# Kernel tuning notes

Hardware: AMD Instinct MI355X
Metric: run time of the kernel (lower is better)

## Reference

```python
import jax, jax.numpy as jnp
import numpy as np

B, S, DIM = 2, 2048, 2048
H, KVH, D = 16, 8, 128
EPS = 1e-6
ROPE_BASE = 1000000.0
MAX_SEQ = 8192


def _build_rope(max_seq, dim, base):
    inv_freq = 1.0 / (base ** (np.arange(0, dim, 2, dtype=np.float64) / dim))
    t = np.arange(max_seq, dtype=np.float64)
    freqs = np.outer(t, inv_freq)  # [max_seq, dim//2]
    return (jnp.asarray(np.cos(freqs), jnp.float32),
            jnp.asarray(np.sin(freqs), jnp.float32))


def setup_inputs() -> dict:
    key = jax.random.key(0)
    ks = jax.random.split(key, 7)
    scale = 0.02
    cos_cache, sin_cache = _build_rope(MAX_SEQ, D, ROPE_BASE)
    return {
        "x": jax.random.normal(ks[0], (B, S, DIM), jnp.float32),
        "wq": jax.random.normal(ks[1], (DIM, H * D), jnp.float32) * scale,
        "wk": jax.random.normal(ks[2], (DIM, KVH * D), jnp.float32) * scale,
        "wv": jax.random.normal(ks[3], (DIM, KVH * D), jnp.float32) * scale,
        "wo": jax.random.normal(ks[4], (H * D, DIM), jnp.float32) * scale,
        "q_gamma": 1.0 + 0.01 * jax.random.normal(ks[5], (D,), jnp.float32),
        "k_gamma": 1.0 + 0.01 * jax.random.normal(ks[6], (D,), jnp.float32),
        "cos_cache": cos_cache,
        "sin_cache": sin_cache,
    }


def _rmsnorm(t, gamma):
    var = jnp.mean(t * t, axis=-1, keepdims=True)
    return t * jax.lax.rsqrt(var + EPS) * gamma


def _rotate_half(t):
    t1, t2 = jnp.split(t, 2, axis=-1)
    return jnp.concatenate((-t2, t1), axis=-1)


def _apply_rope(t, cos, sin):
    # t: [B, S, heads, D]; cos/sin: [S, D//2]
    cos_f = jnp.concatenate((cos, cos), axis=-1)[None, :, None, :]
    sin_f = jnp.concatenate((sin, sin), axis=-1)[None, :, None, :]
    return t * cos_f + _rotate_half(t) * sin_f


def reference(x, wq, wk, wv, wo, q_gamma, k_gamma, cos_cache, sin_cache):
    b, s, _ = x.shape
    q = (x @ wq).reshape(b, s, H, D)
    k = (x @ wk).reshape(b, s, KVH, D)
    v = (x @ wv).reshape(b, s, KVH, D)
    q = _rmsnorm(q, q_gamma)
    k = _rmsnorm(k, k_gamma)
    # prefill: kv_len == q_len == s, cache empty
    cos, sin = cos_cache[:s], sin_cache[:s]
    q = _apply_rope(q, cos, sin)
    k = _apply_rope(k, cos, sin)
    # -> [B, heads, S, D]
    q = q.transpose(0, 2, 1, 3)
    k = k.transpose(0, 2, 1, 3)
    v = v.transpose(0, 2, 1, 3)
    # GQA: repeat_interleave kv heads
    g = H // KVH
    k = jnp.repeat(k, g, axis=1)
    v = jnp.repeat(v, g, axis=1)
    scale = 1.0 / jnp.sqrt(jnp.asarray(D, x.dtype))
    scores = jnp.einsum("bhqd,bhkd->bhqk", q, k) * scale
    causal = jnp.tril(jnp.ones((s, s), bool))
    scores = jnp.where(causal, scores, jnp.finfo(scores.dtype).min)
    attn = jax.nn.softmax(scores, axis=-1)
    out = jnp.einsum("bhqk,bhkd->bhqd", attn, v)
    out = out.transpose(0, 2, 1, 3).reshape(b, s, H * D)
    return out @ wo
```

## Files before the change

kernel.cpp:

```cpp
#include <hip/hip_runtime.h>
#include <hip/hip_bf16.h>


typedef __attribute__((ext_vector_type(8))) short s16x8;
typedef __attribute__((ext_vector_type(4))) float f32x4;
typedef __attribute__((ext_vector_type(16))) float f32x16;

typedef const __attribute__((address_space(1))) void* gas_t;
typedef __attribute__((address_space(3))) void* las_t;
#define GLL16(g, l) __builtin_amdgcn_global_load_lds((gas_t)(const void*)(g), (las_t)(void*)(l), 16, 0, 0)

static __device__ __forceinline__ unsigned short f2bf(float f) {
    union { float f; unsigned u; } v; v.f = f;
    unsigned r = v.u + 0x7FFF + ((v.u >> 16) & 1);
    return (unsigned short)(r >> 16);
}
static __device__ __forceinline__ float bf2f(unsigned short h) {
    union { unsigned u; float f; } v; v.u = ((unsigned)h) << 16;
    return v.f;
}
static __device__ __forceinline__ float exp2_fast(float x) {
    float r; asm("v_exp_f32 %0, %1" : "=v"(r) : "v"(x)); return r;
}
static __device__ __forceinline__ unsigned cvt_pk_bf16(float a, float b) {
    unsigned r; asm("v_cvt_pk_bf16_f32 %0, %1, %2" : "=v"(r) : "v"(a), "v"(b)); return r;
}

#define SCALE_L2E 0.12751744900929f

__global__ __launch_bounds__(256) void k_convert_x(const float* __restrict__ x,
                                                   unsigned short* __restrict__ xb, int n) {
    int i = (blockIdx.x * 256 + threadIdx.x) * 8;
    if (i >= n) return;
    float4 a = *(const float4*)(x + i);
    float4 b = *(const float4*)(x + i + 4);
    s16x8 o;
    o[0] = (short)f2bf(a.x); o[1] = (short)f2bf(a.y); o[2] = (short)f2bf(a.z); o[3] = (short)f2bf(a.w);
    o[4] = (short)f2bf(b.x); o[5] = (short)f2bf(b.y); o[6] = (short)f2bf(b.z); o[7] = (short)f2bf(b.w);
    *(s16x8*)(xb + i) = o;
}

__global__ __launch_bounds__(256) void k_transpose_w(const float* __restrict__ src,
                                                     unsigned short* __restrict__ dst,
                                                     int K, int N, int nbase, int dstld) {
    __shared__ float t[32][33];
    int k0 = blockIdx.x * 32, n0 = blockIdx.y * 32;
    int tx = threadIdx.x & 31, ty0 = threadIdx.x >> 5;
    for (int p = 0; p < 4; p++) {
        int ty = ty0 + p * 8;
        t[ty][tx] = src[(size_t)(k0 + ty) * N + n0 + tx];
    }
    __syncthreads();
    for (int p = 0; p < 4; p++) {
        int ty = ty0 + p * 8;
        dst[(size_t)(nbase + n0 + ty) * dstld + k0 + tx] = f2bf(t[tx][ty]);
    }
}

__global__ __launch_bounds__(256) void k_transpose_v(const unsigned short* __restrict__ V,
                                                     unsigned short* __restrict__ Vt) {
    __shared__ unsigned short t[32][33];
    int s0 = blockIdx.x * 32, d0 = blockIdx.y * 32;
    size_t base = (size_t)blockIdx.z * 2048 * 128;
    int tx = threadIdx.x & 31, ty0 = threadIdx.x >> 5;
    for (int p = 0; p < 4; p++) {
        int ty = ty0 + p * 8;
        t[ty][tx] = V[base + (size_t)(s0 + ty) * 128 + d0 + tx];
    }
    __syncthreads();
    for (int p = 0; p < 4; p++) {
        int ty = ty0 + p * 8;
        Vt[base + (size_t)(d0 + ty) * 2048 + s0 + tx] = t[tx][ty];
    }
}

template<int OUTF32>
__global__ __launch_bounds__(512, 2) void k_gemm256(const unsigned short* __restrict__ A,
                                                    const unsigned short* __restrict__ Bt,
                                                    void* __restrict__ Cout,
                                                    int M, int N, int K) {
    __shared__ unsigned short Ls[2][2][2][8192];
    int tid = threadIdx.x, lane = tid & 63, wave = tid >> 6;
    int wm = wave >> 2, wn = wave & 3;
    int lr = lane & 15, lg = lane >> 4;
    int swrow = wave * 16 + (lane >> 2);
    int scol  = (((lane & 3) ^ ((lane >> 3) & 3)) * 8);
    int cg    = ((lg ^ ((lr >> 1) & 3)) * 8);
    const unsigned short* Ab = A  + (size_t)(blockIdx.x * 256) * K;
    const unsigned short* Bb = Bt + (size_t)(blockIdx.y * 256) * K;

    f32x4 acc[8][4] = {};
    int NK = K / 64;

    auto issue = [&](int slot, int mat, int kk, int k0) {
        const unsigned short* base = mat ? Bb : Ab;
        unsigned short* dst = &Ls[slot][mat][kk][wave * 512];
        GLL16(base + (size_t)swrow * K + k0 + kk * 32 + scol, dst);
        GLL16(base + (size_t)(swrow + 128) * K + k0 + kk * 32 + scol, dst + 4096);
    };

    issue(0, 0, 0, 0);
    issue(0, 1, 0, 0);
    issue(0, 0, 1, 0);
    issue(0, 1, 1, 0);
    asm volatile("s_waitcnt vmcnt(4)" ::: "memory");
    __builtin_amdgcn_s_barrier();

    for (int t = 0; t < NK; ++t) {
        int slot = t & 1, nslot = slot ^ 1;
        int kn = (t + 1) * 64;
        bool more = (t + 1) < NK;
        const unsigned short* As0 = Ls[slot][0][0];
        const unsigned short* Bs0 = Ls[slot][1][0];
        const unsigned short* As1 = Ls[slot][0][1];
        const unsigned short* Bs1 = Ls[slot][1][1];
        s16x8 af[4], bfr[4];

        #pragma unroll
        for (int m = 0; m < 4; m++) af[m]  = *(const s16x8*)&As0[(wm * 128 + m * 16 + lr) * 32 + cg];
        #pragma unroll
        for (int n = 0; n < 4; n++) bfr[n] = *(const s16x8*)&Bs0[(wn * 64 + n * 16 + lr) * 32 + cg];
        if (more) issue(nslot, 0, 0, kn);
        asm volatile("" ::: "memory");
        __builtin_amdgcn_s_barrier();
        __builtin_amdgcn_s_setprio(1);
        #pragma unroll
        for (int m = 0; m < 4; m++)
            #pragma unroll
            for (int n = 0; n < 4; n++)
                acc[m][n] = __builtin_amdgcn_mfma_f32_16x16x32_bf16(af[m], bfr[n], acc[m][n], 0, 0, 0);
        __builtin_amdgcn_s_setprio(0);
        asm volatile("" ::: "memory");
        __builtin_amdgcn_s_barrier();

        #pragma unroll
        for (int m = 0; m < 4; m++) af[m] = *(const s16x8*)&As0[(wm * 128 + (m + 4) * 16 + lr) * 32 + cg];
        if (more) { issue(nslot, 1, 0, kn); asm volatile("s_waitcnt vmcnt(4)" ::: "memory"); }
        else      {                         asm volatile("s_waitcnt vmcnt(0)" ::: "memory"); }
        asm volatile("" ::: "memory");
        __builtin_amdgcn_s_barrier();
        __builtin_amdgcn_s_setprio(1);
        #pragma unroll
        for (int m = 0; m < 4; m++)
            #pragma unroll
            for (int n = 0; n < 4; n++)
                acc[m + 4][n] = __builtin_amdgcn_mfma_f32_16x16x32_bf16(af[m], bfr[n], acc[m + 4][n], 0, 0, 0);
        __builtin_amdgcn_s_setprio(0);
        asm volatile("" ::: "memory");
        __builtin_amdgcn_s_barrier();

        #pragma unroll
        for (int m = 0; m < 4; m++) af[m]  = *(const s16x8*)&As1[(wm * 128 + m * 16 + lr) * 32 + cg];
        #pragma unroll
        for (int n = 0; n < 4; n++) bfr[n] = *(const s16x8*)&Bs1[(wn * 64 + n * 16 + lr) * 32 + cg];
        if (more) issue(nslot, 0, 1, kn);
        asm volatile("" ::: "memory");
        __builtin_amdgcn_s_barrier();
        __builtin_amdgcn_s_setprio(1);
        #pragma unroll
        for (int m = 0; m < 4; m++)
            #pragma unroll
            for (int n = 0; n < 4; n++)
                acc[m][n] = __builtin_amdgcn_mfma_f32_16x16x32_bf16(af[m], bfr[n], acc[m][n], 0, 0, 0);
        __builtin_amdgcn_s_setprio(0);
        asm volatile("" ::: "memory");
        __builtin_amdgcn_s_barrier();

        #pragma unroll
        for (int m = 0; m < 4; m++) af[m] = *(const s16x8*)&As1[(wm * 128 + (m + 4) * 16 + lr) * 32 + cg];
        if (more) { issue(nslot, 1, 1, kn); asm volatile("s_waitcnt vmcnt(4)" ::: "memory"); }
        asm volatile("" ::: "memory");
        __builtin_amdgcn_s_barrier();
        __builtin_amdgcn_s_setprio(1);
        #pragma unroll
        for (int m = 0; m < 4; m++)
            #pragma unroll
            for (int n = 0; n < 4; n++)
                acc[m + 4][n] = __builtin_amdgcn_mfma_f32_16x16x32_bf16(af[m], bfr[n], acc[m + 4][n], 0, 0, 0);
        __builtin_amdgcn_s_setprio(0);
        asm volatile("" ::: "memory");
        __builtin_amdgcn_s_barrier();
    }

    int rbase = blockIdx.x * 256 + wm * 128;
    int cbase = blockIdx.y * 256 + wn * 64;
    #pragma unroll
    for (int am = 0; am < 8; am++)
        #pragma unroll
        for (int n = 0; n < 4; n++)
            #pragma unroll
            for (int r = 0; r < 4; r++) {
                int row = rbase + am * 16 + lg * 4 + r;
                int col = cbase + n * 16 + lr;
                float v = acc[am][n][r];
                if (OUTF32) ((float*)Cout)[(size_t)row * N + col] = v;
                else        ((unsigned short*)Cout)[(size_t)row * N + col] = f2bf(v);
            }
}

template<int OUTF32>
__global__ __launch_bounds__(256) void k_gemm_bt(const unsigned short* __restrict__ A,
                                                 const unsigned short* __restrict__ Bt,
                                                 void* __restrict__ Cout,
                                                 int M, int N, int K) {
    __shared__ unsigned short As[128 * 32];
    __shared__ unsigned short Bs[128 * 32];
    int tid = threadIdx.x;
    int lane = tid & 63;
    int wave = tid >> 6;
    int wm = wave >> 1, wn = wave & 1;
    int lr = lane & 15, lk = (lane >> 4) * 8;
    int srow = wave * 32 + (lane >> 2);
    int scol = (lane & 3) * 8;
    const unsigned short* Ag0 = A  + (size_t)(blockIdx.x * 128 + srow) * K + scol;
    const unsigned short* Ag1 = Ag0 + (size_t)16 * K;
    const unsigned short* Bg0 = Bt + (size_t)(blockIdx.y * 128 + srow) * K + scol;
    const unsigned short* Bg1 = Bg0 + (size_t)16 * K;
    unsigned short* Asw = &As[wave * 1024];
    unsigned short* Bsw = &Bs[wave * 1024];
    f32x4 acc[4][4] = {};
    for (int k0 = 0; k0 < K; k0 += 32) {
        __syncthreads();
        GLL16(Ag0 + k0, Asw);
        GLL16(Ag1 + k0, Asw + 512);
        GLL16(Bg0 + k0, Bsw);
        GLL16(Bg1 + k0, Bsw + 512);
        __syncthreads();
        s16x8 af[4], bfr[4];
        #pragma unroll
        for (int m = 0; m < 4; m++) af[m]  = *(const s16x8*)&As[(wm * 64 + m * 16 + lr) * 32 + lk];
        #pragma unroll
        for (int n = 0; n < 4; n++) bfr[n] = *(const s16x8*)&Bs[(wn * 64 + n * 16 + lr) * 32 + lk];
        #pragma unroll
        for (int m = 0; m < 4; m++)
            #pragma unroll
            for (int n = 0; n < 4; n++)
                acc[m][n] = __builtin_amdgcn_mfma_f32_16x16x32_bf16(af[m], bfr[n], acc[m][n], 0, 0, 0);
    }
    int rbase = blockIdx.x * 128 + wm * 64;
    int cbase = blockIdx.y * 128 + wn * 64;
    #pragma unroll
    for (int m = 0; m < 4; m++)
        #pragma unroll
        for (int n = 0; n < 4; n++)
            #pragma unroll
            for (int r = 0; r < 4; r++) {
                int row = rbase + m * 16 + (lane >> 4) * 4 + r;
                int col = cbase + n * 16 + lr;
                float v = acc[m][n][r];
                if (OUTF32) ((float*)Cout)[(size_t)row * N + col] = v;
                else        ((unsigned short*)Cout)[(size_t)row * N + col] = f2bf(v);
            }
}

__global__ __launch_bounds__(256) void k_rms_rope(const unsigned short* __restrict__ qkv,
                                                  const float* __restrict__ qg,
                                                  const float* __restrict__ kg,
                                                  const float* __restrict__ cosc,
                                                  const float* __restrict__ sinc,
                                                  unsigned short* __restrict__ Qt,
                                                  unsigned short* __restrict__ Kt,
                                                  unsigned short* __restrict__ Vt) {
    int r = blockIdx.x;
    int b = r >> 11;
    int s = r & 2047;
    int tid = threadIdx.x;
    int wave = tid >> 6, lane = tid & 63;
    int sl = lane >> 4;
    int li = lane & 15;
    int d0 = li * 8;
    const unsigned short* row = qkv + (size_t)r * 4096;
    #pragma unroll
    for (int p = 0; p < 2; p++) {
        int seg = p * 16 + wave * 4 + sl;
        s16x8 raw = *(const s16x8*)(row + seg * 128 + d0);
        if (seg >= 24) {
            *(s16x8*)(Vt + ((size_t)(b * 8 + (seg - 24)) * 2048 + s) * 128 + d0) = raw;
            continue;
        }
        float e[8];
        #pragma unroll
        for (int j = 0; j < 8; j++) e[j] = bf2f((unsigned short)raw[j]);
        float ssq = 0.f;
        #pragma unroll
        for (int j = 0; j < 8; j++) ssq += e[j] * e[j];
        ssq += __shfl_xor(ssq, 1, 64);
        ssq += __shfl_xor(ssq, 2, 64);
        ssq += __shfl_xor(ssq, 4, 64);
        ssq += __shfl_xor(ssq, 8, 64);
        float rn = rsqrtf(ssq * (1.0f / 128.0f) + 1e-6f);
        const float* g = (seg < 16) ? qg : kg;
        float gs = (seg < 16) ? SCALE_L2E : 1.0f;
        float4 g0 = *(const float4*)(g + d0);
        float4 g1 = *(const float4*)(g + d0 + 4);
        float t[8];
        t[0] = e[0] * rn * g0.x * gs; t[1] = e[1] * rn * g0.y * gs;
        t[2] = e[2] * rn * g0.z * gs; t[3] = e[3] * rn * g0.w * gs;
        t[4] = e[4] * rn * g1.x * gs; t[5] = e[5] * rn * g1.y * gs;
        t[6] = e[6] * rn * g1.z * gs; t[7] = e[7] * rn * g1.w * gs;
        float pr[8];
        #pragma unroll
        for (int j = 0; j < 8; j++) pr[j] = __shfl_xor(t[j], 8, 64);
        int didx = d0 & 63;
        float4 c0 = *(const float4*)(cosc + (size_t)s * 64 + didx);
        float4 c1 = *(const float4*)(cosc + (size_t)s * 64 + didx + 4);
        float4 sn0 = *(const float4*)(sinc + (size_t)s * 64 + didx);
        float4 sn1 = *(const float4*)(sinc + (size_t)s * 64 + didx + 4);
        float cv[8] = {c0.x, c0.y, c0.z, c0.w, c1.x, c1.y, c1.z, c1.w};
        float sv[8] = {sn0.x, sn0.y, sn0.z, sn0.w, sn1.x, sn1.y, sn1.z, sn1.w};
        float sgn = (li < 8) ? -1.0f : 1.0f;
        s16x8 o;
        #pragma unroll
        for (int j = 0; j < 8; j++)
            o[j] = (short)f2bf(t[j] * cv[j] + sgn * pr[j] * sv[j]);
        unsigned short* dst = (seg < 16)
            ? Qt + ((size_t)(b * 16 + seg) * 2048 + s) * 128 + d0
            : Kt + ((size_t)(b * 8 + (seg - 16)) * 2048 + s) * 128 + d0;
        *(s16x8*)dst = o;
    }
}

__global__ __launch_bounds__(256, 2) void k_attn(const unsigned short* __restrict__ Qt,
                                                 const unsigned short* __restrict__ Kt,
                                                 const unsigned short* __restrict__ Vtg,
                                                 unsigned short* __restrict__ attn) {
    __shared__ unsigned short Ks[64][136];
    __shared__ unsigned short Vs[128][72];
    __shared__ unsigned short Ps[4][32][72];
    int bid = blockIdx.x;
    int lo = bid & 255;
    int qb, bh;
    if (bid < 256) { qb = lo & 15;        bh = lo >> 4; }
    else           { qb = 15 - (lo & 15); bh = 16 + (lo >> 4); }
    int b = bh >> 4, h = bh & 15;
    int kvh = h >> 1;
    int tid = threadIdx.x;
    int lane = tid & 63, wave = tid >> 6;
    int ql = lane & 31;
    int hf = lane >> 5;
    int q0 = qb * 128;
    const unsigned short* Qb    = Qt + ((size_t)bh * 2048 + q0 + wave * 32 + ql) * 128;
    const unsigned short* Kbase = Kt + (size_t)(b * 8 + kvh) * 2048 * 128;
    const unsigned short* Vtb   = Vtg + (size_t)(b * 8 + kvh) * 128 * 2048;
    s16x8 aq[8];
    #pragma unroll
    for (int ds = 0; ds < 8; ds++)
        aq[ds] = *(const s16x8*)(Qb + ds * 16 + hf * 8);
    f32x16 out[4] = {};
    float m_q = -1e30f, l_q = 0.f;
    int qglob = q0 + wave * 32 + ql;
    int qlo   = q0 + wave * 32;
    int qhi   = qlo + 31;
    int ntiles = 2 * qb + 2;
    int krow = tid >> 4, kcol = (tid & 15) * 8;
    int vrow = tid >> 3, vcol = (tid & 7) * 8;
    s16x8 kpre[4], vpre[4];
    #pragma unroll
    for (int p = 0; p < 4; p++) {
        kpre[p] = *(const s16x8*)(Kbase + (size_t)(krow + p * 16) * 128 + kcol);
        vpre[p] = *(const s16x8*)(Vtb + (size_t)(vrow + p * 32) * 2048 + vcol);
    }

    for (int t = 0; t < ntiles; t++) {
        int k0 = t * 64;
        __syncthreads();
        #pragma unroll
        for (int p = 0; p < 4; p++) {
            *(s16x8*)&Ks[krow + p * 16][kcol] = kpre[p];
            *(s16x8*)&Vs[vrow + p * 32][vcol] = vpre[p];
        }
        __syncthreads();
        if (t + 1 < ntiles) {
            int kn = k0 + 64;
            #pragma unroll
            for (int p = 0; p < 4; p++) {
                kpre[p] = *(const s16x8*)(Kbase + (size_t)(kn + krow + p * 16) * 128 + kcol);
                vpre[p] = *(const s16x8*)(Vtb + (size_t)(vrow + p * 32) * 2048 + kn + vcol);
            }
        }
        if (k0 <= qhi) {
            f32x16 st[2] = {};
            __builtin_amdgcn_s_setprio(1);
            #pragma unroll
            for (int sub = 0; sub < 2; sub++)
                #pragma unroll
                for (int ds = 0; ds < 8; ds++) {
                    s16x8 kf = *(const s16x8*)&Ks[sub * 32 + ql][ds * 16 + hf * 8];
                    st[sub] = __builtin_amdgcn_mfma_f32_32x32x16_bf16(kf, aq[ds], st[sub], 0, 0, 0);
                }
            __builtin_amdgcn_s_setprio(0);
            float mx = -1e30f;
            if (k0 + 63 > qlo) {
                #pragma unroll
                for (int sub = 0; sub < 2; sub++)
                    #pragma unroll
                    for (int r = 0; r < 16; r++) {
                        int kv = k0 + sub * 32 + (r & 3) + 8 * (r >> 2) + 4 * hf;
                        if (kv > qglob) st[sub][r] = -1e30f;
                        mx = fmaxf(mx, st[sub][r]);
                    }
            } else {
                #pragma unroll
                for (int sub = 0; sub < 2; sub++)
                    #pragma unroll
                    for (int r = 0; r < 16; r++) mx = fmaxf(mx, st[sub][r]);
            }
            mx = fmaxf(mx, __shfl_xor(mx, 32, 64));
            bool defer = __all(mx <= m_q + 8.0f);
            float sf = 1.0f;
            if (!defer) {
                float mnew = fmaxf(m_q, mx);
                sf = exp2_fast(m_q - mnew);
                m_q = mnew;
            }
            float rs = 0.f;
            #pragma unroll
            for (int sub = 0; sub < 2; sub++)
                #pragma unroll
                for (int r = 0; r < 16; r++) {
                    float e = exp2_fast(st[sub][r] - m_q);
                    st[sub][r] = e;
                    rs += e;
                }
            rs += __shfl_xor(rs, 32, 64);
            l_q = defer ? (l_q + rs) : (l_q * sf + rs);
            #pragma unroll
            for (int sub = 0; sub < 2; sub++)
                #pragma unroll
                for (int g = 0; g < 4; g++) {
                    uint2 w;
                    w.x = cvt_pk_bf16(st[sub][4 * g + 0], st[sub][4 * g + 1]);
                    w.y = cvt_pk_bf16(st[sub][4 * g + 2], st[sub][4 * g + 3]);
                    *(uint2*)&Ps[wave][ql][sub * 32 + g * 8 + hf * 4] = w;
                }
            if (!defer) {
                float sfr[16];
                #pragma unroll
                for (int r = 0; r < 16; r++)
                    sfr[r] = __shfl(sf, (r & 3) + 8 * (r >> 2) + 4 * hf, 64);
                #pragma unroll
                for (int dblk = 0; dblk < 4; dblk++)
                    #pragma unroll
                    for (int r = 0; r < 16; r++) out[dblk][r] *= sfr[r];
            }
            __builtin_amdgcn_s_setprio(1);
            #pragma unroll
            for (int ks = 0; ks < 4; ks++) {
                s16x8 pf = *(const s16x8*)&Ps[wave][ql][ks * 16 + hf * 8];
                #pragma unroll
                for (int dblk = 0; dblk < 4; dblk++) {
                    s16x8 vf = *(const s16x8*)&Vs[dblk * 32 + ql][ks * 16 + hf * 8];
                    out[dblk] = __builtin_amdgcn_mfma_f32_32x32x16_bf16(pf, vf, out[dblk], 0, 0, 0);
                }
            }
            __builtin_amdgcn_s_setprio(0);
        }
    }
    float linv = 1.0f / l_q;
    float inv[16];
    #pragma unroll
    for (int r = 0; r < 16; r++)
        inv[r] = __shfl(linv, (r & 3) + 8 * (r >> 2) + 4 * hf, 64);
    #pragma unroll
    for (int dblk = 0; dblk < 4; dblk++)
        #pragma unroll
        for (int r = 0; r < 16; r++) {
            int row = q0 + wave * 32 + (r & 3) + 8 * (r >> 2) + 4 * hf;
            attn[((size_t)(b * 2048) + row) * 2048 + h * 128 + dblk * 32 + ql] =
                f2bf(out[dblk][r] * inv[r]);
        }
}

extern "C" void kernel_launch(void* const* d_in, const int* in_sizes, int n_in,
                              void* d_out, int out_size, void* d_ws, size_t ws_size,
                              hipStream_t stream) {
    const float* x    = (const float*)d_in[0];
    const float* wq   = (const float*)d_in[1];
    const float* wk   = (const float*)d_in[2];
    const float* wv   = (const float*)d_in[3];
    const float* wo   = (const float*)d_in[4];
    const float* qg   = (const float*)d_in[5];
    const float* kg   = (const float*)d_in[6];
    const float* cosc = (const float*)d_in[7];
    const float* sinc = (const float*)d_in[8];

    char* ws = (char*)d_ws;
    unsigned short* xb   = (unsigned short*)(ws);
    unsigned short* w1t  = (unsigned short*)(ws + 16777216);
    unsigned short* w2t  = (unsigned short*)(ws + 33554432);
    unsigned short* qkv  = (unsigned short*)(ws + 41943040);
    unsigned short* Qt   = (unsigned short*)(ws + 75497472);
    unsigned short* Kt   = (unsigned short*)(ws + 92274688);
    unsigned short* Vt   = (unsigned short*)(ws + 100663296);
    unsigned short* attn = (unsigned short*)(ws + 109051904);
    unsigned short* Vtg  = qkv;

    k_convert_x<<<4096, 256, 0, stream>>>(x, xb, 8388608);
    k_transpose_w<<<dim3(64, 64), 256, 0, stream>>>(wq, w1t, 2048, 2048, 0, 2048);
    k_transpose_w<<<dim3(64, 32), 256, 0, stream>>>(wk, w1t, 2048, 1024, 2048, 2048);
    k_transpose_w<<<dim3(64, 32), 256, 0, stream>>>(wv, w1t, 2048, 1024, 3072, 2048);
    k_transpose_w<<<dim3(64, 64), 256, 0, stream>>>(wo, w2t, 2048, 2048, 0, 2048);
    k_gemm256<0><<<dim3(16, 16), 512, 0, stream>>>(xb, w1t, qkv, 4096, 4096, 2048);
    k_rms_rope<<<4096, 256, 0, stream>>>(qkv, qg, kg, cosc, sinc, Qt, Kt, Vt);
    k_transpose_v<<<dim3(64, 4, 16), 256, 0, stream>>>(Vt, Vtg);
    k_attn<<<512, 256, 0, stream>>>(Qt, Kt, Vtg, attn);
    k_gemm_bt<1><<<dim3(32, 16), 256, 0, stream>>>(attn, w2t, d_out, 4096, 2048, 2048);
}
```

Before: 226.8 us.

## Split attention into single-wave blocks loading K/V straight to registers

Restructures the attention kernel so each block is one 64-thread wave handling 32 queries, launching 2048 blocks instead of 512. K and V fragments are now loaded directly from global memory into registers with software prefetch, which removes the shared-memory staging and block-wide barriers. The block index mapping is also changed to interleave heads and order query chunks in a snake pattern for load balance and L2 locality. The trade-off is losing K/V reuse across the four waves that shared a tile, so global/L2 traffic rises and register pressure goes up from the 16-register K prefetch.

```diff
diff --git a/kernel.cpp b/kernel.cpp
--- a/kernel.cpp
+++ b/kernel.cpp
@@ -320,26 +320,23 @@
     }
 }
 
-__global__ __launch_bounds__(256, 2) void k_attn(const unsigned short* __restrict__ Qt,
-                                                 const unsigned short* __restrict__ Kt,
-                                                 const unsigned short* __restrict__ Vtg,
-                                                 unsigned short* __restrict__ attn) {
-    __shared__ unsigned short Ks[64][136];
-    __shared__ unsigned short Vs[128][72];
-    __shared__ unsigned short Ps[4][32][72];
+__global__ __launch_bounds__(64, 2) void k_attn(const unsigned short* __restrict__ Qt,
+                                                const unsigned short* __restrict__ Kt,
+                                                const unsigned short* __restrict__ Vtg,
+                                                unsigned short* __restrict__ attn) {
+    __shared__ unsigned short Ps[32][72];
     int bid = blockIdx.x;
-    int lo = bid & 255;
-    int qb, bh;
-    if (bid < 256) { qb = lo & 15;        bh = lo >> 4; }
-    else           { qb = 15 - (lo & 15); bh = 16 + (lo >> 4); }
+    int x = bid & 7, l = bid >> 3;
+    int bh = x * 4 + (l & 3);
+    int cc = (l >> 2) & 7, j = l >> 5;
+    int qc = j * 8 + ((j & 1) ? (7 - cc) : cc);
     int b = bh >> 4, h = bh & 15;
     int kvh = h >> 1;
-    int tid = threadIdx.x;
-    int lane = tid & 63, wave = tid >> 6;
+    int lane = threadIdx.x;
     int ql = lane & 31;
     int hf = lane >> 5;
-    int q0 = qb * 128;
-    const unsigned short* Qb    = Qt + ((size_t)bh * 2048 + q0 + wave * 32 + ql) * 128;
+    int q0 = qc * 32;
+    const unsigned short* Qb    = Qt + ((size_t)bh * 2048 + q0 + ql) * 128;
     const unsigned short* Kbase = Kt + (size_t)(b * 8 + kvh) * 2048 * 128;
     const unsigned short* Vtb   = Vtg + (size_t)(b * 8 + kvh) * 128 * 2048;
     s16x8 aq[8];
@@ -348,113 +345,115 @@
         aq[ds] = *(const s16x8*)(Qb + ds * 16 + hf * 8);
     f32x16 out[4] = {};
     float m_q = -1e30f, l_q = 0.f;
-    int qglob = q0 + wave * 32 + ql;
-    int qlo   = q0 + wave * 32;
-    int qhi   = qlo + 31;
-    int ntiles = 2 * qb + 2;
-    int krow = tid >> 4, kcol = (tid & 15) * 8;
-    int vrow = tid >> 3, vcol = (tid & 7) * 8;
-    s16x8 kpre[4], vpre[4];
-    #pragma unroll
-    for (int p = 0; p < 4; p++) {
-        kpre[p] = *(const s16x8*)(Kbase + (size_t)(krow + p * 16) * 128 + kcol);
-        vpre[p] = *(const s16x8*)(Vtb + (size_t)(vrow + p * 32) * 2048 + vcol);
-    }
+    int qglob = q0 + ql;
+    int ntiles = (qc >> 1) + 1;
+    s16x8 kreg[16];
+    #pragma unroll
+    for (int sub = 0; sub < 2; sub++)
+        #pragma unroll
+        for (int ds = 0; ds < 8; ds++)
+            kreg[sub * 8 + ds] = *(const s16x8*)(Kbase + (size_t)(sub * 32 + ql) * 128 + ds * 16 + hf * 8);
 
     for (int t = 0; t < ntiles; t++) {
         int k0 = t * 64;
-        __syncthreads();
-        #pragma unroll
-        for (int p = 0; p < 4; p++) {
-            *(s16x8*)&Ks[krow + p * 16][kcol] = kpre[p];
-            *(s16x8*)&Vs[vrow + p * 32][vcol] = vpre[p];
-        }
-        __syncthreads();
+        f32x16 st[2] = {};
+        __builtin_amdgcn_s_setprio(1);
+        #pragma unroll
+        for (int sub = 0; sub < 2; sub++)
+            #pragma unroll
+            for (int ds = 0; ds < 8; ds++)
+                st[sub] = __builtin_amdgcn_mfma_f32_32x32x16_bf16(kreg[sub * 8 + ds], aq[ds], st[sub], 0, 0, 0);
+        __builtin_amdgcn_s_setprio(0);
         if (t + 1 < ntiles) {
             int kn = k0 + 64;
             #pragma unroll
-            for (int p = 0; p < 4; p++) {
-                kpre[p] = *(const s16x8*)(Kbase + (size_t)(kn + krow + p * 16) * 128 + kcol);
-                vpre[p] = *(const s16x8*)(Vtb + (size_t)(vrow + p * 32) * 2048 + kn + vcol);
-            }
-        }
-        if (k0 <= qhi) {
-            f32x16 st[2] = {};
-            __builtin_amdgcn_s_setprio(1);
-            #pragma unroll
             for (int sub = 0; sub < 2; sub++)
                 #pragma unroll
-                for (int ds = 0; ds < 8; ds++) {
-                    s16x8 kf = *(const s16x8*)&Ks[sub * 32 + ql][ds * 16 + hf * 8];
-                    st[sub] = __builtin_amdgcn_mfma_f32_32x32x16_bf16(kf, aq[ds], st[sub], 0, 0, 0);
-                }
-            __builtin_amdgcn_s_setprio(0);
-            float mx = -1e30f;
-            if (k0 + 63 > qlo) {
-                #pragma unroll
-                for (int sub = 0; sub < 2; sub++)
-                    #pragma unroll
-                    for (int r = 0; r < 16; r++) {
-                        int kv = k0 + sub * 32 + (r & 3) + 8 * (r >> 2) + 4 * hf;
-                        if (kv > qglob) st[sub][r] = -1e30f;
-                        mx = fmaxf(mx, st[sub][r]);
-                    }
-            } else {
-                #pragma unroll
-                for (int sub = 0; sub < 2; sub++)
-                    #pragma unroll
-                    for (int r = 0; r < 16; r++) mx = fmaxf(mx, st[sub][r]);
-            }
-            mx = fmaxf(mx, __shfl_xor(mx, 32, 64));
-            bool defer = __all(mx <= m_q + 8.0f);
-            float sf = 1.0f;
-            if (!defer) {
-                float mnew = fmaxf(m_q, mx);
-                sf = exp2_fast(m_q - mnew);
-                m_q = mnew;
-            }
-            float rs = 0.f;
+                for (int ds = 0; ds < 8; ds++)
+                    kreg[sub * 8 + ds] = *(const s16x8*)(Kbase + (size_t)(kn + sub * 32 + ql) * 128 + ds * 16 + hf * 8);
+        }
+        s16x8 vA[8];
+        #pragma unroll
+        for (int ks = 0; ks < 2; ks++)
+            #pragma unroll
+            for (int dblk = 0; dblk < 4; dblk++)
+                vA[ks * 4 + dblk] = *(const s16x8*)(Vtb + (size_t)(dblk * 32 + ql) * 2048 + k0 + ks * 16 + hf * 8);
+        float mx = -1e30f;
+        if (k0 + 63 > q0) {
             #pragma unroll
             for (int sub = 0; sub < 2; sub++)
                 #pragma unroll
                 for (int r = 0; r < 16; r++) {
-                    float e = exp2_fast(st[sub][r] - m_q);
-                    st[sub][r] = e;
-                    rs += e;
+                    int kv = k0 + sub * 32 + (r & 3) + 8 * (r >> 2) + 4 * hf;
+                    if (kv > qglob) st[sub][r] = -1e30f;
+                    mx = fmaxf(mx, st[sub][r]);
                 }
-            rs += __shfl_xor(rs, 32, 64);
-            l_q = defer ? (l_q + rs) : (l_q * sf + rs);
+        } else {
             #pragma unroll
             for (int sub = 0; sub < 2; sub++)
                 #pragma unroll
-                for (int g = 0; g < 4; g++) {
-                    uint2 w;
-                    w.x = cvt_pk_bf16(st[sub][4 * g + 0], st[sub][4 * g + 1]);
-                    w.y = cvt_pk_bf16(st[sub][4 * g + 2], st[sub][4 * g + 3]);
-                    *(uint2*)&Ps[wave][ql][sub * 32 + g * 8 + hf * 4] = w;
-                }
-            if (!defer) {
-                float sfr[16];
+                for (int r = 0; r < 16; r++) mx = fmaxf(mx, st[sub][r]);
+        }
+        mx = fmaxf(mx, __shfl_xor(mx, 32, 64));
+        bool defer = __all(mx <= m_q + 8.0f);
+        float sf = 1.0f;
+        if (!defer) {
+            float mnew = fmaxf(m_q, mx);
+            sf = exp2_fast(m_q - mnew);
+            m_q = mnew;
+        }
+        float rs = 0.f;
+        #pragma unroll
+        for (int sub = 0; sub < 2; sub++)
+            #pragma unroll
+            for (int r = 0; r < 16; r++) {
+                float e = exp2_fast(st[sub][r] - m_q);
+                st[sub][r] = e;
+                rs += e;
+            }
+        rs += __shfl_xor(rs, 32, 64);
+        l_q = defer ? (l_q + rs) : (l_q * sf + rs);
+        #pragma unroll
+        for (int sub = 0; sub < 2; sub++)
+            #pragma unroll
+            for (int g = 0; g < 4; g++) {
+                uint2 w;
+                w.x = cvt_pk_bf16(st[sub][4 * g + 0], st[sub][4 * g + 1]);
+                w.y = cvt_pk_bf16(st[sub][4 * g + 2], st[sub][4 * g + 3]);
+                *(uint2*)&Ps[ql][sub * 32 + g * 8 + hf * 4] = w;
+            }
+        s16x8 vB[8];
+        #pragma unroll
+        for (int ks = 0; ks < 2; ks++)
+            #pragma unroll
+            for (int dblk = 0; dblk < 4; dblk++)
+                vB[ks * 4 + dblk] = *(const s16x8*)(Vtb + (size_t)(dblk * 32 + ql) * 2048 + k0 + (ks + 2) * 16 + hf * 8);
+        if (!defer) {
+            float sfr[16];
+            #pragma unroll
+            for (int r = 0; r < 16; r++)
+                sfr[r] = __shfl(sf, (r & 3) + 8 * (r >> 2) + 4 * hf, 64);
+            #pragma unroll
+            for (int dblk = 0; dblk < 4; dblk++)
                 #pragma unroll
-                for (int r = 0; r < 16; r++)
-                    sfr[r] = __shfl(sf, (r & 3) + 8 * (r >> 2) + 4 * hf, 64);
-                #pragma unroll
-                for (int dblk = 0; dblk < 4; dblk++)
-                    #pragma unroll
-                    for (int r = 0; r < 16; r++) out[dblk][r] *= sfr[r];
-            }
-            __builtin_amdgcn_s_setprio(1);
-            #pragma unroll
-            for (int ks = 0; ks < 4; ks++) {
-                s16x8 pf = *(const s16x8*)&Ps[wave][ql][ks * 16 + hf * 8];
-                #pragma unroll
-                for (int dblk = 0; dblk < 4; dblk++) {
-                    s16x8 vf = *(const s16x8*)&Vs[dblk * 32 + ql][ks * 16 + hf * 8];
-                    out[dblk] = __builtin_amdgcn_mfma_f32_32x32x16_bf16(pf, vf, out[dblk], 0, 0, 0);
-                }
-            }
-            __builtin_amdgcn_s_setprio(0);
-        }
+                for (int r = 0; r < 16; r++) out[dblk][r] *= sfr[r];
+        }
+        __builtin_amdgcn_s_setprio(1);
+        #pragma unroll
+        for (int ks = 0; ks < 2; ks++) {
+            s16x8 pf = *(const s16x8*)&Ps[ql][ks * 16 + hf * 8];
+            #pragma unroll
+            for (int dblk = 0; dblk < 4; dblk++)
+                out[dblk] = __builtin_amdgcn_mfma_f32_32x32x16_bf16(pf, vA[ks * 4 + dblk], out[dblk], 0, 0, 0);
+        }
+        #pragma unroll
+        for (int ks = 0; ks < 2; ks++) {
+            s16x8 pf = *(const s16x8*)&Ps[ql][(ks + 2) * 16 + hf * 8];
+            #pragma unroll
+            for (int dblk = 0; dblk < 4; dblk++)
+                out[dblk] = __builtin_amdgcn_mfma_f32_32x32x16_bf16(pf, vB[ks * 4 + dblk], out[dblk], 0, 0, 0);
+        }
+        __builtin_amdgcn_s_setprio(0);
     }
     float linv = 1.0f / l_q;
     float inv[16];
@@ -465,7 +464,7 @@
     for (int dblk = 0; dblk < 4; dblk++)
         #pragma unroll
         for (int r = 0; r < 16; r++) {
-            int row = q0 + wave * 32 + (r & 3) + 8 * (r >> 2) + 4 * hf;
+            int row = q0 + (r & 3) + 8 * (r >> 2) + 4 * hf;
             attn[((size_t)(b * 2048) + row) * 2048 + h * 128 + dblk * 32 + ql] =
                 f2bf(out[dblk][r] * inv[r]);
         }
@@ -503,6 +502,6 @@
     k_gemm256<0><<<dim3(16, 16), 512, 0, stream>>>(xb, w1t, qkv, 4096, 4096, 2048);
     k_rms_rope<<<4096, 256, 0, stream>>>(qkv, qg, kg, cosc, sinc, Qt, Kt, Vt);
     k_transpose_v<<<dim3(64, 4, 16), 256, 0, stream>>>(Vt, Vtg);
-    k_attn<<<512, 256, 0, stream>>>(Qt, Kt, Vtg, attn);
+    k_attn<<<2048, 64, 0, stream>>>(Qt, Kt, Vtg, attn);
     k_gemm_bt<1><<<dim3(32, 16), 256, 0, stream>>>(attn, w2t, d_out, 4096, 2048, 2048);
 }
```

Result: slower. 297.2 us (+31.0%).

## Use 4-stage LDS ring in QKV GEMM and merge weight transposes into one launch

Applied to the files above, without the earlier changes.

The 256x256 GEMM moves from a double-buffered 64-wide K step with four barrier-separated phases to a four-slot ring of 32-wide K slices. Loads are issued three slices ahead, and there are two barriers per 32-wide slice. This is meant to hide global-load latency better and cut synchronisation per unit of work. The four weight-transpose launches are merged into one 3D-grid launch, with early exit for the shorter wk and wv matrices, to save launch overhead. The ring keeps the same total LDS, but its vmcnt accounting is more intricate and easier to get wrong.

```diff
diff --git a/kernel.cpp b/kernel.cpp
--- a/kernel.cpp
+++ b/kernel.cpp
@@ -40,11 +40,21 @@
     *(s16x8*)(xb + i) = o;
 }
 
-__global__ __launch_bounds__(256) void k_transpose_w(const float* __restrict__ src,
-                                                     unsigned short* __restrict__ dst,
-                                                     int K, int N, int nbase, int dstld) {
+__global__ __launch_bounds__(256) void k_transpose_w4(const float* __restrict__ wq,
+                                                      const float* __restrict__ wk,
+                                                      const float* __restrict__ wv,
+                                                      const float* __restrict__ wo,
+                                                      unsigned short* __restrict__ w1t,
+                                                      unsigned short* __restrict__ w2t) {
     __shared__ float t[32][33];
+    int z = blockIdx.z;
+    const float* src; unsigned short* dst; int N, nbase;
+    if (z == 0)      { src = wq; dst = w1t; N = 2048; nbase = 0;    }
+    else if (z == 1) { src = wk; dst = w1t; N = 1024; nbase = 2048; }
+    else if (z == 2) { src = wv; dst = w1t; N = 1024; nbase = 3072; }
+    else             { src = wo; dst = w2t; N = 2048; nbase = 0;    }
     int k0 = blockIdx.x * 32, n0 = blockIdx.y * 32;
+    if (n0 >= N) return;
     int tx = threadIdx.x & 31, ty0 = threadIdx.x >> 5;
     for (int p = 0; p < 4; p++) {
         int ty = ty0 + p * 8;
@@ -53,7 +63,7 @@
     __syncthreads();
     for (int p = 0; p < 4; p++) {
         int ty = ty0 + p * 8;
-        dst[(size_t)(nbase + n0 + ty) * dstld + k0 + tx] = f2bf(t[tx][ty]);
+        dst[(size_t)(nbase + n0 + ty) * 2048 + k0 + tx] = f2bf(t[tx][ty]);
     }
 }
 
@@ -79,7 +89,7 @@
                                                     const unsigned short* __restrict__ Bt,
                                                     void* __restrict__ Cout,
                                                     int M, int N, int K) {
-    __shared__ unsigned short Ls[2][2][2][8192];
+    __shared__ unsigned short Ls[4 * 2 * 8192];
     int tid = threadIdx.x, lane = tid & 63, wave = tid >> 6;
     int wm = wave >> 2, wn = wave & 3;
     int lr = lane & 15, lg = lane >> 4;
@@ -90,39 +100,41 @@
     const unsigned short* Bb = Bt + (size_t)(blockIdx.y * 256) * K;
 
     f32x4 acc[8][4] = {};
-    int NK = K / 64;
-
-    auto issue = [&](int slot, int mat, int kk, int k0) {
+    int NK = K / 32;
+
+    auto issue = [&](int ring, int mat, int k0) {
         const unsigned short* base = mat ? Bb : Ab;
-        unsigned short* dst = &Ls[slot][mat][kk][wave * 512];
-        GLL16(base + (size_t)swrow * K + k0 + kk * 32 + scol, dst);
-        GLL16(base + (size_t)(swrow + 128) * K + k0 + kk * 32 + scol, dst + 4096);
+        unsigned short* dst = &Ls[(ring * 2 + mat) * 8192 + wave * 512];
+        GLL16(base + (size_t)swrow * K + k0 + scol, dst);
+        GLL16(base + (size_t)(swrow + 128) * K + k0 + scol, dst + 4096);
     };
 
-    issue(0, 0, 0, 0);
-    issue(0, 1, 0, 0);
-    issue(0, 0, 1, 0);
-    issue(0, 1, 1, 0);
-    asm volatile("s_waitcnt vmcnt(4)" ::: "memory");
+    issue(0, 0, 0);  issue(0, 1, 0);
+    issue(1, 0, 32); issue(1, 1, 32);
+    issue(2, 0, 64); issue(2, 1, 64);
+    asm volatile("s_waitcnt vmcnt(8)" ::: "memory");
     __builtin_amdgcn_s_barrier();
+    asm volatile("" ::: "memory");
 
     for (int t = 0; t < NK; ++t) {
-        int slot = t & 1, nslot = slot ^ 1;
-        int kn = (t + 1) * 64;
-        bool more = (t + 1) < NK;
-        const unsigned short* As0 = Ls[slot][0][0];
-        const unsigned short* Bs0 = Ls[slot][1][0];
-        const unsigned short* As1 = Ls[slot][0][1];
-        const unsigned short* Bs1 = Ls[slot][1][1];
+        int ring = t & 3;
+        const unsigned short* As = &Ls[(ring * 2 + 0) * 8192];
+        const unsigned short* Bs = &Ls[(ring * 2 + 1) * 8192];
         s16x8 af[4], bfr[4];
-
-        #pragma unroll
-        for (int m = 0; m < 4; m++) af[m]  = *(const s16x8*)&As0[(wm * 128 + m * 16 + lr) * 32 + cg];
-        #pragma unroll
-        for (int n = 0; n < 4; n++) bfr[n] = *(const s16x8*)&Bs0[(wn * 64 + n * 16 + lr) * 32 + cg];
-        if (more) issue(nslot, 0, 0, kn);
+        #pragma unroll
+        for (int m = 0; m < 4; m++) af[m]  = *(const s16x8*)&As[(wm * 128 + m * 16 + lr) * 32 + cg];
+        #pragma unroll
+        for (int n = 0; n < 4; n++) bfr[n] = *(const s16x8*)&Bs[(wn * 64 + n * 16 + lr) * 32 + cg];
+        int rem = NK - 1 - t;
+        if (rem >= 3) {
+            int kn = (t + 3) * 32, rn = (t + 3) & 3;
+            issue(rn, 0, kn); issue(rn, 1, kn);
+        }
+        if (rem >= 3)      asm volatile("s_waitcnt vmcnt(8)" ::: "memory");
+        else if (rem == 2) asm volatile("s_waitcnt vmcnt(4)" ::: "memory");
+        else if (rem == 1) asm volatile("s_waitcnt vmcnt(0)" ::: "memory");
+        __builtin_amdgcn_s_barrier();
         asm volatile("" ::: "memory");
-        __builtin_amdgcn_s_barrier();
         __builtin_amdgcn_s_setprio(1);
         #pragma unroll
         for (int m = 0; m < 4; m++)
@@ -130,15 +142,8 @@
             for (int n = 0; n < 4; n++)
                 acc[m][n] = __builtin_amdgcn_mfma_f32_16x16x32_bf16(af[m], bfr[n], acc[m][n], 0, 0, 0);
         __builtin_amdgcn_s_setprio(0);
-        asm volatile("" ::: "memory");
-        __builtin_amdgcn_s_barrier();
-
-        #pragma unroll
-        for (int m = 0; m < 4; m++) af[m] = *(const s16x8*)&As0[(wm * 128 + (m + 4) * 16 + lr) * 32 + cg];
-        if (more) { issue(nslot, 1, 0, kn); asm volatile("s_waitcnt vmcnt(4)" ::: "memory"); }
-        else      {                         asm volatile("s_waitcnt vmcnt(0)" ::: "memory"); }
-        asm volatile("" ::: "memory");
-        __builtin_amdgcn_s_barrier();
+        #pragma unroll
+        for (int m = 0; m < 4; m++) af[m] = *(const s16x8*)&As[(wm * 128 + (m + 4) * 16 + lr) * 32 + cg];
         __builtin_amdgcn_s_setprio(1);
         #pragma unroll
         for (int m = 0; m < 4; m++)
@@ -148,38 +153,7 @@
         __builtin_amdgcn_s_setprio(0);
         asm volatile("" ::: "memory");
         __builtin_amdgcn_s_barrier();
-
-        #pragma unroll
-        for (int m = 0; m < 4; m++) af[m]  = *(const s16x8*)&As1[(wm * 128 + m * 16 + lr) * 32 + cg];
-        #pragma unroll
-        for (int n = 0; n < 4; n++) bfr[n] = *(const s16x8*)&Bs1[(wn * 64 + n * 16 + lr) * 32 + cg];
-        if (more) issue(nslot, 0, 1, kn);
         asm volatile("" ::: "memory");
-        __builtin_amdgcn_s_barrier();
-        __builtin_amdgcn_s_setprio(1);
-        #pragma unroll
-        for (int m = 0; m < 4; m++)
-            #pragma unroll
-            for (int n = 0; n < 4; n++)
-                acc[m][n] = __builtin_amdgcn_mfma_f32_16x16x32_bf16(af[m], bfr[n], acc[m][n], 0, 0, 0);
-        __builtin_amdgcn_s_setprio(0);
-        asm volatile("" ::: "memory");
-        __builtin_amdgcn_s_barrier();
-
-        #pragma unroll
-        for (int m = 0; m < 4; m++) af[m] = *(const s16x8*)&As1[(wm * 128 + (m + 4) * 16 + lr) * 32 + cg];
-        if (more) { issue(nslot, 1, 1, kn); asm volatile("s_waitcnt vmcnt(4)" ::: "memory"); }
-        asm volatile("" ::: "memory");
-        __builtin_amdgcn_s_barrier();
-        __builtin_amdgcn_s_setprio(1);
-        #pragma unroll
-        for (int m = 0; m < 4; m++)
-            #pragma unroll
-            for (int n = 0; n < 4; n++)
-                acc[m + 4][n] = __builtin_amdgcn_mfma_f32_16x16x32_bf16(af[m], bfr[n], acc[m + 4][n], 0, 0, 0);
-        __builtin_amdgcn_s_setprio(0);
-        asm volatile("" ::: "memory");
-        __builtin_amdgcn_s_barrier();
     }
 
     int rbase = blockIdx.x * 256 + wm * 128;
@@ -496,10 +470,7 @@
     unsigned short* Vtg  = qkv;
 
     k_convert_x<<<4096, 256, 0, stream>>>(x, xb, 8388608);
-    k_transpose_w<<<dim3(64, 64), 256, 0, stream>>>(wq, w1t, 2048, 2048, 0, 2048);
-    k_transpose_w<<<dim3(64, 32), 256, 0, stream>>>(wk, w1t, 2048, 1024, 2048, 2048);
-    k_transpose_w<<<dim3(64, 32), 256, 0, stream>>>(wv, w1t, 2048, 1024, 3072, 2048);
-    k_transpose_w<<<dim3(64, 64), 256, 0, stream>>>(wo, w2t, 2048, 2048, 0, 2048);
+    k_transpose_w4<<<dim3(64, 64, 4), 256, 0, stream>>>(wq, wk, wv, wo, w1t, w2t);
     k_gemm256<0><<<dim3(16, 16), 512, 0, stream>>>(xb, w1t, qkv, 4096, 4096, 2048);
     k_rms_rope<<<4096, 256, 0, stream>>>(qkv, qg, kg, cosc, sinc, Qt, Kt, Vt);
     k_transpose_v<<<dim3(64, 4, 16), 256, 0, stream>>>(Vt, Vtg);
```

Result: no change. 223.2 us (-1.6%).

## Swizzle attention LDS tiles, double-buffer K/V, merge weight transposes into one launch

Applied to the files above, without the earlier changes.

The attention kernel's K, V and P shared-memory tiles drop their row padding and use an XOR swizzle on 16-byte chunks to avoid bank conflicts. K/V tiles are double-buffered, which removes one of the two barriers per KV tile. The four weight-transpose launches are merged into a single launch indexed by blockIdx.z, with early exit for the out-of-range blocks of the narrower K/V weights. Double buffering doubles the K/V LDS footprint, which may affect occupancy at two blocks per CU.

```diff
diff --git a/kernel.cpp b/kernel.cpp
--- a/kernel.cpp
+++ b/kernel.cpp
@@ -40,11 +40,21 @@
     *(s16x8*)(xb + i) = o;
 }
 
-__global__ __launch_bounds__(256) void k_transpose_w(const float* __restrict__ src,
-                                                     unsigned short* __restrict__ dst,
-                                                     int K, int N, int nbase, int dstld) {
+__global__ __launch_bounds__(256) void k_transpose_w4(const float* __restrict__ wq,
+                                                      const float* __restrict__ wk,
+                                                      const float* __restrict__ wv,
+                                                      const float* __restrict__ wo,
+                                                      unsigned short* __restrict__ w1t,
+                                                      unsigned short* __restrict__ w2t) {
     __shared__ float t[32][33];
+    int z = blockIdx.z;
+    const float* src; unsigned short* dst; int N, nbase;
+    if (z == 0)      { src = wq; dst = w1t; N = 2048; nbase = 0;    }
+    else if (z == 1) { src = wk; dst = w1t; N = 1024; nbase = 2048; }
+    else if (z == 2) { src = wv; dst = w1t; N = 1024; nbase = 3072; }
+    else             { src = wo; dst = w2t; N = 2048; nbase = 0;    }
     int k0 = blockIdx.x * 32, n0 = blockIdx.y * 32;
+    if (n0 >= N) return;
     int tx = threadIdx.x & 31, ty0 = threadIdx.x >> 5;
     for (int p = 0; p < 4; p++) {
         int ty = ty0 + p * 8;
@@ -53,7 +63,7 @@
     __syncthreads();
     for (int p = 0; p < 4; p++) {
         int ty = ty0 + p * 8;
-        dst[(size_t)(nbase + n0 + ty) * dstld + k0 + tx] = f2bf(t[tx][ty]);
+        dst[(size_t)(nbase + n0 + ty) * 2048 + k0 + tx] = f2bf(t[tx][ty]);
     }
 }
 
@@ -324,9 +334,9 @@
                                                  const unsigned short* __restrict__ Kt,
                                                  const unsigned short* __restrict__ Vtg,
                                                  unsigned short* __restrict__ attn) {
-    __shared__ unsigned short Ks[64][136];
-    __shared__ unsigned short Vs[128][72];
-    __shared__ unsigned short Ps[4][32][72];
+    __shared__ unsigned short Ks[2][64 * 128];
+    __shared__ unsigned short Vs[2][128 * 64];
+    __shared__ unsigned short Ps[4][32 * 64];
     int bid = blockIdx.x;
     int lo = bid & 255;
     int qb, bh;
@@ -352,30 +362,33 @@
     int qlo   = q0 + wave * 32;
     int qhi   = qlo + 31;
     int ntiles = 2 * qb + 2;
-    int krow = tid >> 4, kcol = (tid & 15) * 8;
-    int vrow = tid >> 3, vcol = (tid & 7) * 8;
+    int krow = tid >> 4, kcolb = tid & 15;
+    int vrow = tid >> 3, vcolb = tid & 7;
+    int ksw = kcolb ^ (krow & 7);
+    int vsw = vcolb ^ (vrow & 7);
+    int eq = (ql & 7);
     s16x8 kpre[4], vpre[4];
     #pragma unroll
     for (int p = 0; p < 4; p++) {
-        kpre[p] = *(const s16x8*)(Kbase + (size_t)(krow + p * 16) * 128 + kcol);
-        vpre[p] = *(const s16x8*)(Vtb + (size_t)(vrow + p * 32) * 2048 + vcol);
+        kpre[p] = *(const s16x8*)(Kbase + (size_t)(krow + p * 16) * 128 + kcolb * 8);
+        vpre[p] = *(const s16x8*)(Vtb + (size_t)(vrow + p * 32) * 2048 + vcolb * 8);
     }
 
     for (int t = 0; t < ntiles; t++) {
         int k0 = t * 64;
-        __syncthreads();
+        int buf = t & 1;
         #pragma unroll
         for (int p = 0; p < 4; p++) {
-            *(s16x8*)&Ks[krow + p * 16][kcol] = kpre[p];
-            *(s16x8*)&Vs[vrow + p * 32][vcol] = vpre[p];
+            *(s16x8*)&Ks[buf][(krow + p * 16) * 128 + ksw * 8] = kpre[p];
+            *(s16x8*)&Vs[buf][(vrow + p * 32) * 64  + vsw * 8] = vpre[p];
         }
         __syncthreads();
         if (t + 1 < ntiles) {
             int kn = k0 + 64;
             #pragma unroll
             for (int p = 0; p < 4; p++) {
-                kpre[p] = *(const s16x8*)(Kbase + (size_t)(kn + krow + p * 16) * 128 + kcol);
-                vpre[p] = *(const s16x8*)(Vtb + (size_t)(vrow + p * 32) * 2048 + kn + vcol);
+                kpre[p] = *(const s16x8*)(Kbase + (size_t)(kn + krow + p * 16) * 128 + kcolb * 8);
+                vpre[p] = *(const s16x8*)(Vtb + (size_t)(vrow + p * 32) * 2048 + kn + vcolb * 8);
             }
         }
         if (k0 <= qhi) {
@@ -385,7 +398,7 @@
             for (int sub = 0; sub < 2; sub++)
                 #pragma unroll
                 for (int ds = 0; ds < 8; ds++) {
-                    s16x8 kf = *(const s16x8*)&Ks[sub * 32 + ql][ds * 16 + hf * 8];
+                    s16x8 kf = *(const s16x8*)&Ks[buf][(sub * 32 + ql) * 128 + ((ds * 2 + hf) ^ eq) * 8];
                     st[sub] = __builtin_amdgcn_mfma_f32_32x32x16_bf16(kf, aq[ds], st[sub], 0, 0, 0);
                 }
             __builtin_amdgcn_s_setprio(0);
@@ -431,7 +444,7 @@
                     uint2 w;
                     w.x = cvt_pk_bf16(st[sub][4 * g + 0], st[sub][4 * g + 1]);
                     w.y = cvt_pk_bf16(st[sub][4 * g + 2], st[sub][4 * g + 3]);
-                    *(uint2*)&Ps[wave][ql][sub * 32 + g * 8 + hf * 4] = w;
+                    *(uint2*)&Ps[wave][ql * 64 + ((sub * 8 + g * 2 + hf) ^ (eq << 1)) * 4] = w;
                 }
             if (!defer) {
                 float sfr[16];
@@ -446,10 +459,10 @@
             __builtin_amdgcn_s_setprio(1);
             #pragma unroll
             for (int ks = 0; ks < 4; ks++) {
-                s16x8 pf = *(const s16x8*)&Ps[wave][ql][ks * 16 + hf * 8];
+                s16x8 pf = *(const s16x8*)&Ps[wave][ql * 64 + ((ks * 4 + hf * 2) ^ (eq << 1)) * 4];
                 #pragma unroll
                 for (int dblk = 0; dblk < 4; dblk++) {
-                    s16x8 vf = *(const s16x8*)&Vs[dblk * 32 + ql][ks * 16 + hf * 8];
+                    s16x8 vf = *(const s16x8*)&Vs[buf][(dblk * 32 + ql) * 64 + ((ks * 2 + hf) ^ eq) * 8];
                     out[dblk] = __builtin_amdgcn_mfma_f32_32x32x16_bf16(pf, vf, out[dblk], 0, 0, 0);
                 }
             }
@@ -496,10 +509,7 @@
     unsigned short* Vtg  = qkv;
 
     k_convert_x<<<4096, 256, 0, stream>>>(x, xb, 8388608);
-    k_transpose_w<<<dim3(64, 64), 256, 0, stream>>>(wq, w1t, 2048, 2048, 0, 2048);
-    k_transpose_w<<<dim3(64, 32), 256, 0, stream>>>(wk, w1t, 2048, 1024, 2048, 2048);
-    k_transpose_w<<<dim3(64, 32), 256, 0, stream>>>(wv, w1t, 2048, 1024, 3072, 2048);
-    k_transpose_w<<<dim3(64, 64), 256, 0, stream>>>(wo, w2t, 2048, 2048, 0, 2048);
+    k_transpose_w4<<<dim3(64, 64, 4), 256, 0, stream>>>(wq, wk, wv, wo, w1t, w2t);
     k_gemm256<0><<<dim3(16, 16), 512, 0, stream>>>(xb, w1t, qkv, 4096, 4096, 2048);
     k_rms_rope<<<4096, 256, 0, stream>>>(qkv, qg, kg, cosc, sinc, Qt, Kt, Vt);
     k_transpose_v<<<dim3(64, 4, 16), 256, 0, stream>>>(Vt, Vtg);
```

Result: no change. 226.5 us (-0.1%).
